# Performance work log

Hardware: AMD Instinct MI355X
Metric: run time of the kernel (lower is better)

## Reference

```python
import jax, jax.numpy as jnp
import numpy as np

B, L, D = 2, 1024, 2048
E, K = 8, 2
H, HS = 1408, 2816


def setup_inputs() -> dict:
    key = jax.random.key(0)
    ks = jax.random.split(key, 9)
    s = 0.02  # param init scale
    return {
        "x": jax.random.normal(ks[0], (B, L, D), dtype=jnp.float32),
        "gate_w": jax.random.normal(ks[1], (E, D), dtype=jnp.float32) * s,
        "w_gate": jax.random.normal(ks[2], (E, D, H), dtype=jnp.float32) * s,
        "w_up": jax.random.normal(ks[3], (E, D, H), dtype=jnp.float32) * s,
        "w_down": jax.random.normal(ks[4], (E, H, D), dtype=jnp.float32) * s,
        "shgate_w": jax.random.normal(ks[5], (D,), dtype=jnp.float32) * s,
        "shw_gate": jax.random.normal(ks[6], (D, HS), dtype=jnp.float32) * s,
        "shw_up": jax.random.normal(ks[7], (D, HS), dtype=jnp.float32) * s,
        "shw_down": jax.random.normal(ks[8], (HS, D), dtype=jnp.float32) * s,
    }


def reference(x, gate_w, w_gate, w_up, w_down, shgate_w, shw_gate, shw_up, shw_down):
    b, l, d = x.shape
    xf = x.reshape(-1, d)  # [T, D]

    # --- router: softmax over expert logits, top-k, renormalize ---
    logits = jnp.einsum("td,ed->te", xf.astype(jnp.float32), gate_w)
    probs = jax.nn.softmax(logits.astype(jnp.float32), axis=-1)  # [T, E]
    weights, indices = jax.lax.top_k(probs, K)                   # [T, K]
    weights = (weights / weights.sum(-1, keepdims=True)).astype(x.dtype)

    # per-token combine weight for each expert: sum of top-k weights routed to e
    onehot = jax.nn.one_hot(indices, E, dtype=x.dtype)           # [T, K, E]
    combine = jnp.einsum("tk,tke->te", weights, onehot)          # [T, E]

    # --- experts (dense vectorized equivalent of masked gather/scatter loop) ---
    g = jnp.einsum("td,edh->teh", xf, w_gate)
    u = jnp.einsum("td,edh->teh", xf, w_up)
    h = jax.nn.silu(g) * u                                       # [T, E, H]
    # fused down-proj + weighted combine; accumulate in fp32 like the original
    out = jnp.einsum("teh,ehd,te->td", h.astype(jnp.float32),
                     w_down.astype(jnp.float32), combine.astype(jnp.float32))

    # --- shared expert with sigmoid gate ---
    sgate = jax.nn.sigmoid(xf @ shgate_w)[:, None]               # [T, 1]
    sh = (jax.nn.silu(xf @ shw_gate) * (xf @ shw_up)) @ shw_down  # [T, D]
    out = out + (sgate * sh).astype(jnp.float32)

    return out.astype(x.dtype).reshape(b, l, d)
```

## Files before the change

kernel.cpp:

```cpp
#include <hip/hip_runtime.h>
#include <hip/hip_bf16.h>
#include <math.h>

#define T_TOK 2048
#define Dd    2048
#define Ee    8
#define Hh    1408
#define HSs   2816
#define CAP   1024

typedef __attribute__((ext_vector_type(8))) __bf16 bf16x8;
typedef __attribute__((ext_vector_type(4))) __bf16 bf16x4;
typedef __attribute__((ext_vector_type(4))) float  f32x4;

#define MFMA(a, b, c) __builtin_amdgcn_mfma_f32_16x16x32_bf16(a, b, c, 0, 0, 0)

__device__ __forceinline__ void async_copy16(const __bf16* g, __bf16* l) {
    __builtin_amdgcn_global_load_lds(
        (const __attribute__((address_space(1))) unsigned int*)g,
        (__attribute__((address_space(3))) unsigned int*)l, 16, 0, 0);
}


__global__ void init_cnt(int* __restrict__ cnt) {
    if (threadIdx.x < Ee) cnt[threadIdx.x] = 0;
}

__global__ __launch_bounds__(256) void router_kernel(
    const float* __restrict__ x, const float* __restrict__ gate_w,
    const float* __restrict__ shgate_w,
    int* __restrict__ cnt, int* __restrict__ ptok,
    int* __restrict__ slot, float* __restrict__ swt,
    float* __restrict__ sgate, __bf16* __restrict__ xb)
{
    const int t = blockIdx.x;
    const int tid = threadIdx.x;
    const float* xt = x + (size_t)t * Dd;

    float acc[Ee];
#pragma unroll
    for (int e = 0; e < Ee; e++) acc[e] = 0.f;
    float accs = 0.f;

    for (int d = tid; d < Dd; d += 256) {
        float xv = xt[d];
        xb[(size_t)t * Dd + d] = (__bf16)xv;
#pragma unroll
        for (int e = 0; e < Ee; e++) acc[e] += xv * gate_w[e * Dd + d];
        accs += xv * shgate_w[d];
    }

    __shared__ float red[Ee + 1][256];
#pragma unroll
    for (int e = 0; e < Ee; e++) red[e][tid] = acc[e];
    red[Ee][tid] = accs;
    __syncthreads();

    for (int s = 128; s > 0; s >>= 1) {
        if (tid < s) {
#pragma unroll
            for (int e = 0; e <= Ee; e++) red[e][tid] += red[e][tid + s];
        }
        __syncthreads();
    }

    if (tid == 0) {
        float l0 = -1e30f, l1 = -1e30f;
        int i0 = 0, i1 = 0;
#pragma unroll
        for (int e = 0; e < Ee; e++) {
            float v = red[e][0];
            if (v > l0) { l1 = l0; i1 = i0; l0 = v; i0 = e; }
            else if (v > l1) { l1 = v; i1 = e; }
        }
        float w0 = 1.f / (1.f + expf(l1 - l0));
        float w1 = 1.f - w0;

        int p0 = atomicAdd(&cnt[i0], 1);
        if (p0 < CAP) { ptok[i0 * CAP + p0] = t; slot[t * 2] = i0 * CAP + p0; swt[t * 2] = w0; }
        else          { slot[t * 2] = 0; swt[t * 2] = 0.f; }
        int p1 = atomicAdd(&cnt[i1], 1);
        if (p1 < CAP) { ptok[i1 * CAP + p1] = t; slot[t * 2 + 1] = i1 * CAP + p1; swt[t * 2 + 1] = w1; }
        else          { slot[t * 2 + 1] = 0; swt[t * 2 + 1] = 0.f; }

        sgate[t] = 1.f / (1.f + expf(-red[Ee][0]));
    }
}

__global__ __launch_bounds__(256) void transpose_cvt(
    const float* __restrict__ src, __bf16* __restrict__ dst, int R, int C)
{
    const size_t bstride = (size_t)R * C;
    src += blockIdx.z * bstride;
    dst += blockIdx.z * bstride;
    __shared__ float tile[32][33];
    const int tx = threadIdx.x, ty = threadIdx.y;
    const int c0 = blockIdx.x * 32, r0 = blockIdx.y * 32;
#pragma unroll
    for (int j = 0; j < 4; j++)
        tile[ty + 8 * j][tx] = src[(size_t)(r0 + ty + 8 * j) * C + c0 + tx];
    __syncthreads();
    const int tid = ty * 32 + tx;
    const int cc = tid >> 3, r4 = (tid & 7) * 4;
    bf16x4 o = { (__bf16)tile[r4 + 0][cc], (__bf16)tile[r4 + 1][cc],
                 (__bf16)tile[r4 + 2][cc], (__bf16)tile[r4 + 3][cc] };
    *(bf16x4*)(dst + (size_t)(c0 + cc) * R + r0 + r4) = o;
}

#define GU_SH_BLOCKS ((T_TOK / 128) * (HSs / 64))
#define GU_EX_BLOCKS (Ee * 8 * (Hh / 64))

__global__ __launch_bounds__(256, 3) void gateup_all(
    const __bf16* __restrict__ xb,
    const __bf16* __restrict__ wgT, const __bf16* __restrict__ wuT,
    const __bf16* __restrict__ swgT, const __bf16* __restrict__ swuT,
    const int* __restrict__ cnt, const int* __restrict__ ptok,
    __bf16* __restrict__ hq, __bf16* __restrict__ shh)
{
    const int tid = threadIdx.x, lane = tid & 63, wave = tid >> 6;
    __shared__ __align__(16) __bf16 As[2][128 * 32];
    __shared__ __align__(16) __bf16 Bg[2][64 * 32];
    __shared__ __align__(16) __bf16 Bu[2][64 * 32];
    __shared__ int tok_s[128];

    const int bid = blockIdx.x;
    const int kq = (((tid & 3) ^ ((tid >> 3) & 3)) * 8);
    const __bf16 *wg, *wu, *ga1, *ga2;
    __bf16* outp;
    int ostride, m0, h0;

    if (bid < GU_SH_BLOCKS) {
        int ht = bid % 44, mt = bid / 44;
        m0 = mt * 128; h0 = ht * 64;
        wg = swgT; wu = swuT;
        outp = shh; ostride = HSs;
        ga1 = xb + (size_t)(m0 + (tid >> 2)) * Dd + kq;
        ga2 = xb + (size_t)(m0 + 64 + (tid >> 2)) * Dd + kq;
    } else {
        int b2 = bid - GU_SH_BLOCKS;
        int em = b2 & 63, ht = b2 >> 6;
        int e = em & 7, mt = em >> 3;
        int n = cnt[e]; if (n > CAP) n = CAP;
        m0 = mt * 128;
        if (m0 >= n) return;
        h0 = ht * 64;
        wg = wgT + (size_t)e * Hh * Dd; wu = wuT + (size_t)e * Hh * Dd;
        outp = hq + (size_t)e * CAP * Hh; ostride = Hh;
        if (tid < 128) {
            int i = m0 + tid; int ic = i < n ? i : n - 1;
            tok_s[tid] = ptok[e * CAP + ic];
        }
        __syncthreads();
        ga1 = xb + (size_t)tok_s[tid >> 2] * Dd + kq;
        ga2 = xb + (size_t)tok_s[64 + (tid >> 2)] * Dd + kq;
    }
    const __bf16* gbg = wg + (size_t)(h0 + (tid >> 2)) * Dd + kq;
    const __bf16* gbu = wu + (size_t)(h0 + (tid >> 2)) * Dd + kq;

    f32x4 accg[2][4] = {}, accu[2][4] = {};
    const int q = lane >> 4, m = lane & 15;
    const int cbr = (q ^ ((m >> 1) & 3)) * 8;

#define GU_STAGE(bb, k0) do {                              \
    async_copy16(ga1 + (k0), As[bb] + tid * 8);            \
    async_copy16(ga2 + (k0), As[bb] + (tid + 256) * 8);    \
    async_copy16(gbg + (k0), Bg[bb] + tid * 8);            \
    async_copy16(gbu + (k0), Bu[bb] + tid * 8); } while (0)

    GU_STAGE(0, 0);
    __syncthreads();
    int cur = 0;
    for (int t = 0; t < Dd / 32; ++t) {
        if (t + 1 < Dd / 32) GU_STAGE(cur ^ 1, (t + 1) * 32);
        bf16x8 af[2], bgf[4], buf_[4];
        af[0] = *(const bf16x8*)(As[cur] + (wave * 32 + m) * 32 + cbr);
        af[1] = *(const bf16x8*)(As[cur] + (wave * 32 + 16 + m) * 32 + cbr);
#pragma unroll
        for (int j = 0; j < 4; j++) {
            bgf[j]  = *(const bf16x8*)(Bg[cur] + (j * 16 + m) * 32 + cbr);
            buf_[j] = *(const bf16x8*)(Bu[cur] + (j * 16 + m) * 32 + cbr);
        }
#pragma unroll
        for (int i = 0; i < 2; i++)
#pragma unroll
            for (int j = 0; j < 4; j++) {
                accg[i][j] = MFMA(af[i], bgf[j], accg[i][j]);
                accu[i][j] = MFMA(af[i], buf_[j], accu[i][j]);
            }
        __syncthreads();
        cur ^= 1;
    }
#undef GU_STAGE

#pragma unroll
    for (int i = 0; i < 2; i++)
#pragma unroll
        for (int r = 0; r < 4; r++) {
            int row = m0 + wave * 32 + i * 16 + q * 4 + r;
#pragma unroll
            for (int j = 0; j < 4; j++) {
                int h = h0 + j * 16 + m;
                float g = accg[i][j][r], u = accu[i][j][r];
                float s = g / (1.f + __expf(-g));
                outp[(size_t)row * ostride + h] = (__bf16)(s * u);
            }
        }
}

#define DN_SH_BLOCKS ((T_TOK / 128) * (Dd / 128))
#define DN_EX_BLOCKS (Ee * 8 * (Dd / 128))

__global__ __launch_bounds__(256, 3) void down_all(
    const __bf16* __restrict__ shh, const __bf16* __restrict__ shwdT,
    const __bf16* __restrict__ hq, const __bf16* __restrict__ wdT,
    const int* __restrict__ cnt, const float* __restrict__ sgate,
    float* __restrict__ out, float* __restrict__ dexp)
{
    const int tid = threadIdx.x, lane = tid & 63, wave = tid >> 6;
    const int wr = wave >> 1, wc = wave & 1;
    __shared__ __align__(16) __bf16 As[2][128 * 32];
    __shared__ __align__(16) __bf16 Bs[2][128 * 32];

    const int bid = blockIdx.x;
    const __bf16 *A, *BT;
    int m0, n0, K, shared_path, arow_base = 0;

    if (bid < DN_SH_BLOCKS) {
        int nt = bid & 15, mt = bid >> 4;
        m0 = mt * 128; n0 = nt * 128; K = HSs;
        A = shh; BT = shwdT; shared_path = 1;
    } else {
        int b2 = bid - DN_SH_BLOCKS;
        int em = b2 & 63, nt = b2 >> 6;
        int e = em & 7, mt = em >> 3;
        int n = cnt[e]; if (n > CAP) n = CAP;
        m0 = mt * 128;
        if (m0 >= n) return;
        n0 = nt * 128; K = Hh;
        A = hq + (size_t)e * CAP * Hh;
        BT = wdT + (size_t)e * Dd * Hh;
        arow_base = e * CAP;
        shared_path = 0;
    }

    const int kq = (((tid & 3) ^ ((tid >> 3) & 3)) * 8);
    const __bf16* ga1 = A + (size_t)(m0 + (tid >> 2)) * K + kq;
    const __bf16* ga2 = A + (size_t)(m0 + 64 + (tid >> 2)) * K + kq;
    const __bf16* gb1 = BT + (size_t)(n0 + (tid >> 2)) * K + kq;
    const __bf16* gb2 = BT + (size_t)(n0 + 64 + (tid >> 2)) * K + kq;

    f32x4 acc[4][4] = {};
    const int q = lane >> 4, m = lane & 15;
    const int cbr = (q ^ ((m >> 1) & 3)) * 8;

#define DN_STAGE(bb, k0) do {                              \
    async_copy16(ga1 + (k0), As[bb] + tid * 8);            \
    async_copy16(ga2 + (k0), As[bb] + (tid + 256) * 8);    \
    async_copy16(gb1 + (k0), Bs[bb] + tid * 8);            \
    async_copy16(gb2 + (k0), Bs[bb] + (tid + 256) * 8); } while (0)

    DN_STAGE(0, 0);
    __syncthreads();
    int cur = 0;
    const int ntk = K / 32;
    for (int t = 0; t < ntk; ++t) {
        if (t + 1 < ntk) DN_STAGE(cur ^ 1, (t + 1) * 32);
        bf16x8 af[4], bf[4];
#pragma unroll
        for (int i = 0; i < 4; i++) {
            af[i] = *(const bf16x8*)(As[cur] + (wr * 64 + i * 16 + m) * 32 + cbr);
            bf[i] = *(const bf16x8*)(Bs[cur] + (wc * 64 + i * 16 + m) * 32 + cbr);
        }
#pragma unroll
        for (int i = 0; i < 4; i++)
#pragma unroll
            for (int j = 0; j < 4; j++)
                acc[i][j] = MFMA(af[i], bf[j], acc[i][j]);
        __syncthreads();
        cur ^= 1;
    }
#undef DN_STAGE

    if (shared_path) {
#pragma unroll
        for (int i = 0; i < 4; i++)
#pragma unroll
            for (int r = 0; r < 4; r++) {
                int trow = m0 + wr * 64 + i * 16 + q * 4 + r;
                float sg = sgate[trow];
#pragma unroll
                for (int j = 0; j < 4; j++)
                    out[(size_t)trow * Dd + n0 + wc * 64 + j * 16 + m] = sg * acc[i][j][r];
            }
    } else {
#pragma unroll
        for (int i = 0; i < 4; i++)
#pragma unroll
            for (int r = 0; r < 4; r++) {
                int row = arow_base + m0 + wr * 64 + i * 16 + q * 4 + r;
#pragma unroll
                for (int j = 0; j < 4; j++)
                    dexp[(size_t)row * Dd + n0 + wc * 64 + j * 16 + m] = acc[i][j][r];
            }
    }
}

__global__ __launch_bounds__(256) void combine_kernel(
    const float* __restrict__ dexp, const int* __restrict__ slot,
    const float* __restrict__ swt, float* __restrict__ out)
{
    const int t = blockIdx.x, tid = threadIdx.x;
    const int s0 = slot[t * 2], s1 = slot[t * 2 + 1];
    const float w0 = swt[t * 2], w1 = swt[t * 2 + 1];
    const float4* d0 = (const float4*)(dexp + (size_t)s0 * Dd);
    const float4* d1 = (const float4*)(dexp + (size_t)s1 * Dd);
    float4* o = (float4*)(out + (size_t)t * Dd);
#pragma unroll
    for (int it = 0; it < 2; ++it) {
        int i = tid + it * 256;
        float4 a = o[i], b0 = d0[i], b1 = d1[i];
        a.x += w0 * b0.x + w1 * b1.x;
        a.y += w0 * b0.y + w1 * b1.y;
        a.z += w0 * b0.z + w1 * b1.z;
        a.w += w0 * b0.w + w1 * b1.w;
        o[i] = a;
    }
}

extern "C" void kernel_launch(void* const* d_in, const int* in_sizes, int n_in,
                              void* d_out, int out_size, void* d_ws, size_t ws_size,
                              hipStream_t stream) {
    const float* x        = (const float*)d_in[0];
    const float* gate_w   = (const float*)d_in[1];
    const float* w_gate   = (const float*)d_in[2];
    const float* w_up     = (const float*)d_in[3];
    const float* w_down   = (const float*)d_in[4];
    const float* shgate_w = (const float*)d_in[5];
    const float* shw_gate = (const float*)d_in[6];
    const float* shw_up   = (const float*)d_in[7];
    const float* shw_down = (const float*)d_in[8];
    float* out = (float*)d_out;

    char* ws = (char*)d_ws;
    size_t off = 0;
    auto alloc = [&](size_t bytes) { char* p = ws + off; off = (off + bytes + 255) & ~(size_t)255; return p; };
    int*    cnt    = (int*)   alloc(Ee * 4);
    int*    ptok   = (int*)   alloc(Ee * CAP * 4);
    int*    slot   = (int*)   alloc(T_TOK * 2 * 4);
    float*  swt    = (float*) alloc(T_TOK * 2 * 4);
    float*  sgate  = (float*) alloc(T_TOK * 4);
    __bf16* xb     = (__bf16*)alloc((size_t)T_TOK * Dd * 2);
    __bf16* wgT    = (__bf16*)alloc((size_t)Ee * Hh * Dd * 2);
    __bf16* wuT    = (__bf16*)alloc((size_t)Ee * Hh * Dd * 2);
    __bf16* wdT    = (__bf16*)alloc((size_t)Ee * Dd * Hh * 2);
    __bf16* shwgT  = (__bf16*)alloc((size_t)HSs * Dd * 2);
    __bf16* shwuT  = (__bf16*)alloc((size_t)HSs * Dd * 2);
    __bf16* shwdT  = (__bf16*)alloc((size_t)Dd * HSs * 2);
    __bf16* hq     = (__bf16*)alloc((size_t)Ee * CAP * Hh * 2);
    __bf16* shh    = (__bf16*)alloc((size_t)T_TOK * HSs * 2);
    float* dexp = (float*)wgT;

    dim3 b256(256), bT(32, 8);

    init_cnt<<<dim3(1), dim3(64), 0, stream>>>(cnt);
    transpose_cvt<<<dim3(Hh / 32, Dd / 32, Ee), bT, 0, stream>>>(w_gate, wgT, Dd, Hh);
    transpose_cvt<<<dim3(Hh / 32, Dd / 32, Ee), bT, 0, stream>>>(w_up, wuT, Dd, Hh);
    transpose_cvt<<<dim3(Dd / 32, Hh / 32, Ee), bT, 0, stream>>>(w_down, wdT, Hh, Dd);
    transpose_cvt<<<dim3(HSs / 32, Dd / 32, 1), bT, 0, stream>>>(shw_gate, shwgT, Dd, HSs);
    transpose_cvt<<<dim3(HSs / 32, Dd / 32, 1), bT, 0, stream>>>(shw_up, shwuT, Dd, HSs);
    transpose_cvt<<<dim3(Dd / 32, HSs / 32, 1), bT, 0, stream>>>(shw_down, shwdT, HSs, Dd);

    router_kernel<<<dim3(T_TOK), b256, 0, stream>>>(x, gate_w, shgate_w,
                                                    cnt, ptok, slot, swt, sgate, xb);

    gateup_all<<<dim3(GU_SH_BLOCKS + GU_EX_BLOCKS), b256, 0, stream>>>(
        xb, wgT, wuT, shwgT, shwuT, cnt, ptok, hq, shh);

    down_all<<<dim3(DN_SH_BLOCKS + DN_EX_BLOCKS), b256, 0, stream>>>(
        shh, shwdT, hq, wdT, cnt, sgate, out, dexp);

    combine_kernel<<<dim3(T_TOK), b256, 0, stream>>>(dexp, slot, swt, out);
}
```

Baseline: 685.7 us.

## Use three-stage LDS pipeline with explicit vmcnt waits in gate-up and down GEMMs

Both the gate/up and down-projection GEMM kernels move from double buffering to a three-buffer ring in LDS. Loads are issued two K-steps ahead, and the full __syncthreads is replaced by a partial s_waitcnt vmcnt plus a raw barrier, so one stage of async global-to-LDS copies stays in flight during compute. This is meant to hide global memory latency better. LDS use rises by half (48KB for down_all), which may limit the 3-blocks-per-CU occupancy target, and the hand-written waitcnt values must match exactly the four copies issued per stage.

```diff
diff --git a/kernel.cpp b/kernel.cpp
--- a/kernel.cpp
+++ b/kernel.cpp
@@ -14,6 +14,10 @@
 typedef __attribute__((ext_vector_type(4))) float  f32x4;
 
 #define MFMA(a, b, c) __builtin_amdgcn_mfma_f32_16x16x32_bf16(a, b, c, 0, 0, 0)
+
+#define VMCNT4() asm volatile("s_waitcnt vmcnt(4)" ::: "memory")
+#define VMCNT0() asm volatile("s_waitcnt vmcnt(0)" ::: "memory")
+#define BAR()    __builtin_amdgcn_s_barrier()
 
 __device__ __forceinline__ void async_copy16(const __bf16* g, __bf16* l) {
     __builtin_amdgcn_global_load_lds(
@@ -118,9 +122,9 @@
     __bf16* __restrict__ hq, __bf16* __restrict__ shh)
 {
     const int tid = threadIdx.x, lane = tid & 63, wave = tid >> 6;
-    __shared__ __align__(16) __bf16 As[2][128 * 32];
-    __shared__ __align__(16) __bf16 Bg[2][64 * 32];
-    __shared__ __align__(16) __bf16 Bu[2][64 * 32];
+    __shared__ __align__(16) __bf16 As[3 * 128 * 32];
+    __shared__ __align__(16) __bf16 Bg[3 * 64 * 32];
+    __shared__ __align__(16) __bf16 Bu[3 * 64 * 32];
     __shared__ int tok_s[128];
 
     const int bid = blockIdx.x;
@@ -161,24 +165,34 @@
     const int q = lane >> 4, m = lane & 15;
     const int cbr = (q ^ ((m >> 1) & 3)) * 8;
 
-#define GU_STAGE(bb, k0) do {                              \
-    async_copy16(ga1 + (k0), As[bb] + tid * 8);            \
-    async_copy16(ga2 + (k0), As[bb] + (tid + 256) * 8);    \
-    async_copy16(gbg + (k0), Bg[bb] + tid * 8);            \
-    async_copy16(gbu + (k0), Bu[bb] + tid * 8); } while (0)
-
+#define GU_STAGE(bb, k0) do {                                  \
+    __bf16* As_ = As + (bb) * (128 * 32);                      \
+    __bf16* Bg_ = Bg + (bb) * (64 * 32);                       \
+    __bf16* Bu_ = Bu + (bb) * (64 * 32);                       \
+    async_copy16(ga1 + (k0), As_ + tid * 8);                   \
+    async_copy16(ga2 + (k0), As_ + (tid + 256) * 8);           \
+    async_copy16(gbg + (k0), Bg_ + tid * 8);                   \
+    async_copy16(gbu + (k0), Bu_ + tid * 8); } while (0)
+
+    const int nt = Dd / 32;
     GU_STAGE(0, 0);
-    __syncthreads();
+    GU_STAGE(1, 32);
+    VMCNT4();
+    BAR();
     int cur = 0;
-    for (int t = 0; t < Dd / 32; ++t) {
-        if (t + 1 < Dd / 32) GU_STAGE(cur ^ 1, (t + 1) * 32);
+    for (int t = 0; t < nt; ++t) {
+        int s2 = cur + 2; if (s2 >= 3) s2 -= 3;
+        if (t + 2 < nt) GU_STAGE(s2, (t + 2) * 32);
+        const __bf16* Asc = As + cur * (128 * 32);
+        const __bf16* Bgc = Bg + cur * (64 * 32);
+        const __bf16* Buc = Bu + cur * (64 * 32);
         bf16x8 af[2], bgf[4], buf_[4];
-        af[0] = *(const bf16x8*)(As[cur] + (wave * 32 + m) * 32 + cbr);
-        af[1] = *(const bf16x8*)(As[cur] + (wave * 32 + 16 + m) * 32 + cbr);
+        af[0] = *(const bf16x8*)(Asc + (wave * 32 + m) * 32 + cbr);
+        af[1] = *(const bf16x8*)(Asc + (wave * 32 + 16 + m) * 32 + cbr);
 #pragma unroll
         for (int j = 0; j < 4; j++) {
-            bgf[j]  = *(const bf16x8*)(Bg[cur] + (j * 16 + m) * 32 + cbr);
-            buf_[j] = *(const bf16x8*)(Bu[cur] + (j * 16 + m) * 32 + cbr);
+            bgf[j]  = *(const bf16x8*)(Bgc + (j * 16 + m) * 32 + cbr);
+            buf_[j] = *(const bf16x8*)(Buc + (j * 16 + m) * 32 + cbr);
         }
 #pragma unroll
         for (int i = 0; i < 2; i++)
@@ -187,8 +201,10 @@
                 accg[i][j] = MFMA(af[i], bgf[j], accg[i][j]);
                 accu[i][j] = MFMA(af[i], buf_[j], accu[i][j]);
             }
-        __syncthreads();
-        cur ^= 1;
+        if (t + 2 < nt)      VMCNT4();
+        else if (t + 1 < nt) VMCNT0();
+        BAR();
+        cur = cur + 1 == 3 ? 0 : cur + 1;
     }
 #undef GU_STAGE
 
@@ -218,8 +234,8 @@
 {
     const int tid = threadIdx.x, lane = tid & 63, wave = tid >> 6;
     const int wr = wave >> 1, wc = wave & 1;
-    __shared__ __align__(16) __bf16 As[2][128 * 32];
-    __shared__ __align__(16) __bf16 Bs[2][128 * 32];
+    __shared__ __align__(16) __bf16 As[3 * 128 * 32];
+    __shared__ __align__(16) __bf16 Bs[3 * 128 * 32];
 
     const int bid = blockIdx.x;
     const __bf16 *A, *BT;
@@ -253,31 +269,40 @@
     const int q = lane >> 4, m = lane & 15;
     const int cbr = (q ^ ((m >> 1) & 3)) * 8;
 
-#define DN_STAGE(bb, k0) do {                              \
-    async_copy16(ga1 + (k0), As[bb] + tid * 8);            \
-    async_copy16(ga2 + (k0), As[bb] + (tid + 256) * 8);    \
-    async_copy16(gb1 + (k0), Bs[bb] + tid * 8);            \
-    async_copy16(gb2 + (k0), Bs[bb] + (tid + 256) * 8); } while (0)
-
+#define DN_STAGE(bb, k0) do {                                  \
+    __bf16* As_ = As + (bb) * (128 * 32);                      \
+    __bf16* Bs_ = Bs + (bb) * (128 * 32);                      \
+    async_copy16(ga1 + (k0), As_ + tid * 8);                   \
+    async_copy16(ga2 + (k0), As_ + (tid + 256) * 8);           \
+    async_copy16(gb1 + (k0), Bs_ + tid * 8);                   \
+    async_copy16(gb2 + (k0), Bs_ + (tid + 256) * 8); } while (0)
+
+    const int ntk = K / 32;
     DN_STAGE(0, 0);
-    __syncthreads();
+    DN_STAGE(1, 32);
+    VMCNT4();
+    BAR();
     int cur = 0;
-    const int ntk = K / 32;
     for (int t = 0; t < ntk; ++t) {
-        if (t + 1 < ntk) DN_STAGE(cur ^ 1, (t + 1) * 32);
+        int s2 = cur + 2; if (s2 >= 3) s2 -= 3;
+        if (t + 2 < ntk) DN_STAGE(s2, (t + 2) * 32);
+        const __bf16* Asc = As + cur * (128 * 32);
+        const __bf16* Bsc = Bs + cur * (128 * 32);
         bf16x8 af[4], bf[4];
 #pragma unroll
         for (int i = 0; i < 4; i++) {
-            af[i] = *(const bf16x8*)(As[cur] + (wr * 64 + i * 16 + m) * 32 + cbr);
-            bf[i] = *(const bf16x8*)(Bs[cur] + (wc * 64 + i * 16 + m) * 32 + cbr);
+            af[i] = *(const bf16x8*)(Asc + (wr * 64 + i * 16 + m) * 32 + cbr);
+            bf[i] = *(const bf16x8*)(Bsc + (wc * 64 + i * 16 + m) * 32 + cbr);
         }
 #pragma unroll
         for (int i = 0; i < 4; i++)
 #pragma unroll
             for (int j = 0; j < 4; j++)
                 acc[i][j] = MFMA(af[i], bf[j], acc[i][j]);
-        __syncthreads();
-        cur ^= 1;
+        if (t + 2 < ntk)      VMCNT4();
+        else if (t + 1 < ntk) VMCNT0();
+        BAR();
+        cur = cur + 1 == 3 ? 0 : cur + 1;
     }
 #undef DN_STAGE
 
```

After: 674.5 us. Within noise of the previous version (-1.6%).
